# Optimization experiments

Measured on AMD Instinct MI355X. Metric: run time of the kernel, lower is better.

The kernel has to match this reference:

```python
import jax, jax.numpy as jnp
import numpy as np

EMB = 768
HEADS = 12
HEAD_DIM = EMB // HEADS
LAMBDA_INIT = 0.5
LN_EPS = 1e-5


def _rope_tables(seq_len, head_dim):
    # theta_j = 10000^{-2j/d}, j = 0..d/2-1 (standard RoPE)
    j = jnp.arange(head_dim // 2, dtype=jnp.float32)
    theta = jnp.power(10000.0, -2.0 * j / head_dim)            # [d/2]
    ang = jnp.arange(seq_len, dtype=jnp.float32)[:, None] * theta[None, :]  # [S, d/2]
    return jnp.cos(ang), jnp.sin(ang)


def _apply_rope(x, cos, sin):
    # x: [B, H, S, D]; cos/sin: [S, D/2]; rotate consecutive pairs (2j, 2j+1)
    x1 = x[..., 0::2]
    x2 = x[..., 1::2]
    c = cos[None, None, :, :]
    s = sin[None, None, :, :]
    r1 = x1 * c - x2 * s
    r2 = x1 * s + x2 * c
    return jnp.stack([r1, r2], axis=-1).reshape(x.shape)


def setup_inputs() -> dict:
    key = jax.random.key(0)
    ks = jax.random.split(key, 10)
    B, S, E = 2, 2048, EMB
    sd = 1.0 / np.sqrt(E)
    return {
        "x": jax.random.normal(ks[0], (B, S, E), jnp.float32),
        "Wq": jax.random.normal(ks[1], (E, 2 * E), jnp.float32) * sd,
        "bq": jnp.zeros((2 * E,), jnp.float32),
        "Wk": jax.random.normal(ks[2], (E, 2 * E), jnp.float32) * sd,
        "bk": jnp.zeros((2 * E,), jnp.float32),
        "Wv": jax.random.normal(ks[3], (E, E), jnp.float32) * sd,
        "bv": jnp.zeros((E,), jnp.float32),
        "Wo": jax.random.normal(ks[4], (E, E), jnp.float32) * sd,
        "bo": jnp.zeros((E,), jnp.float32),
        "q_scale": jnp.ones((1, 1, 2 * E), jnp.float32),
        "k_scale": jnp.ones((1, 1, 2 * E), jnp.float32),
        "v_scale": jnp.ones((1, 1, E), jnp.float32),
        "o_scale": jnp.ones((1, 1, E), jnp.float32),
        "lambda_param": jnp.asarray(0.0, jnp.float32),
    }


def reference(x, Wq, bq, Wk, bk, Wv, bv, Wo, bo,
              q_scale, k_scale, v_scale, o_scale, lambda_param):
    B, S, E = x.shape
    H, D = HEADS, HEAD_DIM

    Q = (x @ Wq + bq) * q_scale          # [B, S, 2E]
    K = (x @ Wk + bk) * k_scale          # [B, S, 2E]
    V = (x @ Wv + bv) * v_scale          # [B, S, E]

    Q1, Q2 = jnp.split(Q, 2, axis=-1)
    K1, K2 = jnp.split(K, 2, axis=-1)

    def to_heads(t):  # [B, S, E] -> [B, H, S, D]
        return t.reshape(B, S, H, D).transpose(0, 2, 1, 3)

    Q1, Q2, K1, K2, Vh = map(to_heads, (Q1, Q2, K1, K2, V))

    cos, sin = _rope_tables(S, D)
    Q1, Q2 = _apply_rope(Q1, cos, sin), _apply_rope(Q2, cos, sin)
    K1, K2 = _apply_rope(K1, cos, sin), _apply_rope(K2, cos, sin)

    scale = 1.0 / jnp.sqrt(jnp.asarray(D, jnp.float32))
    p1 = jax.nn.softmax(jnp.einsum("bhqd,bhkd->bhqk", Q1, K1) * scale, axis=-1)
    p2 = jax.nn.softmax(jnp.einsum("bhqd,bhkd->bhqk", Q2, K2) * scale, axis=-1)

    lam = jax.nn.sigmoid(lambda_param)
    ctx = jnp.einsum("bhqk,bhkd->bhqd", p1 - lam * p2, Vh)  # [B, H, S, D]

    # layer_norm over head_dim, no affine params
    mu = jnp.mean(ctx, axis=-1, keepdims=True)
    var = jnp.mean(jnp.square(ctx - mu), axis=-1, keepdims=True)
    ctx = (ctx - mu) * jax.lax.rsqrt(var + LN_EPS)

    ctx = ctx * (1.0 - LAMBDA_INIT)
    ctx = ctx.transpose(0, 2, 1, 3).reshape(B, S, E)
    return (ctx @ Wo + bo) * o_scale
```

## Files before the change

### kernel.cpp

```cpp
#include <hip/hip_runtime.h>
#include <hip/hip_bf16.h>

#define BB 2
#define SS 2048
#define EE 768
#define HH 12
#define DD 64
#define MM (BB*SS)

typedef __bf16 bf16_t;
typedef __bf16 bf16x8 __attribute__((ext_vector_type(8)));
typedef __bf16 bf16x4 __attribute__((ext_vector_type(4)));
typedef float  f32x4  __attribute__((ext_vector_type(4)));

static __device__ __forceinline__ f32x4 mfma16(bf16x8 a, bf16x8 b, f32x4 c) {
    return __builtin_amdgcn_mfma_f32_16x16x32_bf16(a, b, c, 0, 0, 0);
}

static __device__ __forceinline__ void gload_lds16(const bf16_t* g, bf16_t* l) {
    __builtin_amdgcn_global_load_lds(
        (const __attribute__((address_space(1))) void*)g,
        (__attribute__((address_space(3))) void*)l,
        16, 0, 0);
}

__global__ __launch_bounds__(256)
void prep_kernel(const float* __restrict__ x,
                 const float* __restrict__ Wq, const float* __restrict__ Wk,
                 const float* __restrict__ Wv, const float* __restrict__ Wo,
                 bf16_t* __restrict__ xb,
                 bf16_t* __restrict__ WqT, bf16_t* __restrict__ WkT,
                 bf16_t* __restrict__ WvT, bf16_t* __restrict__ WoT,
                 float* __restrict__ ctab, float* __restrict__ stab)
{
    __shared__ float tile[32][33];
    const int bx = blockIdx.x, tid = threadIdx.x;

    if (bx < 1536) {
        int i = (bx * 256 + tid) * 8;
        float4 a = *reinterpret_cast<const float4*>(x + i);
        float4 b = *reinterpret_cast<const float4*>(x + i + 4);
        bf16x8 v;
        v[0] = (bf16_t)a.x; v[1] = (bf16_t)a.y; v[2] = (bf16_t)a.z; v[3] = (bf16_t)a.w;
        v[4] = (bf16_t)b.x; v[5] = (bf16_t)b.y; v[6] = (bf16_t)b.z; v[7] = (bf16_t)b.w;
        *reinterpret_cast<bf16x8*>(xb + i) = v;
        return;
    }
    if (bx < 1792) {
        int t = (bx - 1536) * 256 + tid;
        int s = t >> 5, j = t & 31;
        float theta = exp2f(-(float)j * (13.287712379549449f / 32.0f));
        float ang = (float)s * theta;
        float sn, cs;
        sincosf(ang, &sn, &cs);
        ctab[t] = cs;
        stab[t] = sn;
        return;
    }
    int idx = bx - 1792;
    const float* W; bf16_t* WT; int N;
    if (idx < 1152)      { W = Wq; WT = WqT; N = 1536; }
    else if (idx < 2304) { W = Wk; WT = WkT; N = 1536; idx -= 1152; }
    else if (idx < 2880) { W = Wv; WT = WvT; N = 768;  idx -= 2304; }
    else                 { W = Wo; WT = WoT; N = 768;  idx -= 2880; }
    const int ntiles = N >> 5;
    const int n0 = (idx % ntiles) * 32, k0 = (idx / ntiles) * 32;
    const int tx = tid & 31, ty = tid >> 5;
    #pragma unroll
    for (int r = 0; r < 32; r += 8)
        tile[ty + r][tx] = W[(size_t)(k0 + ty + r) * N + n0 + tx];
    __syncthreads();
    #pragma unroll
    for (int r = 0; r < 32; r += 8)
        WT[(size_t)(n0 + ty + r) * 768 + k0 + tx] = (bf16_t)tile[tx][ty + r];
}

__global__ __launch_bounds__(256)
void gemm_qkv_kernel(const bf16_t* __restrict__ xb,
                     const bf16_t* __restrict__ WqT, const bf16_t* __restrict__ WkT,
                     const bf16_t* __restrict__ WvT,
                     const float* __restrict__ bq, const float* __restrict__ bk,
                     const float* __restrict__ bv,
                     const float* __restrict__ qs, const float* __restrict__ ks,
                     const float* __restrict__ vs,
                     const float* __restrict__ ctab, const float* __restrict__ stab,
                     bf16_t* __restrict__ Qr, bf16_t* __restrict__ Kr, bf16_t* __restrict__ Vt)
{
    __shared__ __align__(16) bf16_t As[128 * 64];
    __shared__ __align__(16) bf16_t Bs[128 * 64];
    const int tid = threadIdx.x;
    const int w = tid >> 6, lane = tid & 63, q15 = lane & 15, g = lane >> 4;
    const int m0 = blockIdx.x * 128;
    const int nt = blockIdx.y;

    const bf16_t* Wsrc; const float* bias; const float* scale;
    int nloc0, mode; bf16_t* dstQK = nullptr; float qmul = 1.0f;
    if (nt < 12)      { Wsrc = WqT; bias = bq; scale = qs; nloc0 = nt * 128;        mode = 0; dstQK = Qr;
                        qmul = 0.125f * 1.4426950408889634f; }
    else if (nt < 24) { Wsrc = WkT; bias = bk; scale = ks; nloc0 = (nt - 12) * 128; mode = 0; dstQK = Kr; }
    else              { Wsrc = WvT; bias = bv; scale = vs; nloc0 = (nt - 24) * 128; mode = 1; }

    f32x4 acc[4][4];
    #pragma unroll
    for (int i = 0; i < 4; ++i)
        #pragma unroll
        for (int j = 0; j < 4; ++j)
            acc[i][j] = f32x4{0.f, 0.f, 0.f, 0.f};

    const bf16_t* gA[4]; const bf16_t* gB[4]; bf16_t* lA[4]; bf16_t* lB[4];
    #pragma unroll
    for (int c = 0; c < 4; ++c) {
        int t16 = c * 256 + tid;
        int row = t16 >> 3;
        int sc16 = (t16 & 7) ^ (row & 7);
        gA[c] = &xb[(size_t)(m0 + row) * 768 + sc16 * 8];
        gB[c] = &Wsrc[(size_t)(nloc0 + row) * 768 + sc16 * 8];
        lA[c] = &As[(c * 256 + w * 64) * 8];
        lB[c] = &Bs[(c * 256 + w * 64) * 8];
    }

    const int ar0 = (w >> 1) * 64, bc0 = (w & 1) * 64;
    const int xr = q15 & 7;

    for (int k0 = 0; k0 < 768; k0 += 64) {
        if (k0) __syncthreads();
        #pragma unroll
        for (int c = 0; c < 4; ++c) {
            gload_lds16(gA[c] + k0, lA[c]);
            gload_lds16(gB[c] + k0, lB[c]);
        }
        __syncthreads();
        #pragma unroll
        for (int st = 0; st < 2; ++st) {
            const int cA = ((4 * st + g) ^ xr) * 8;
            bf16x8 af[4], bfr[4];
            #pragma unroll
            for (int i = 0; i < 4; ++i)
                af[i] = *reinterpret_cast<const bf16x8*>(&As[(ar0 + i * 16 + q15) * 64 + cA]);
            #pragma unroll
            for (int j = 0; j < 4; ++j)
                bfr[j] = *reinterpret_cast<const bf16x8*>(&Bs[(bc0 + j * 16 + q15) * 64 + cA]);
            #pragma unroll
            for (int i = 0; i < 4; ++i)
                #pragma unroll
                for (int j = 0; j < 4; ++j)
                    acc[i][j] = mfma16(af[i], bfr[j], acc[i][j]);
        }
    }

    const int mbase = m0 + (w >> 1) * 64;
    const int nbase = nloc0 + (w & 1) * 64;
    #pragma unroll
    for (int j = 0; j < 4; ++j) {
        const int n = nbase + j * 16 + q15;
        const float bi = bias[n];
        const float sc = scale[n] * qmul;
        if (mode == 1) {
            const int h = n >> 6, d = n & 63;
            #pragma unroll
            for (int i = 0; i < 4; ++i)
                #pragma unroll
                for (int r = 0; r < 4; ++r) {
                    int m = mbase + i * 16 + g * 4 + r;
                    int b = m >> 11, s = m & 2047;
                    float v = (acc[i][j][r] + bi) * sc;
                    Vt[((size_t)(b * HH + h) * DD + d) * SS + s] = (bf16_t)v;
                }
        } else {
            const int br = (n >= 768) ? 1 : 0;
            const int n2 = n - br * 768;
            const int h = n2 >> 6, d = n2 & 63, jj = d >> 1;
            #pragma unroll
            for (int i = 0; i < 4; ++i)
                #pragma unroll
                for (int r = 0; r < 4; ++r) {
                    int m = mbase + i * 16 + g * 4 + r;
                    int b = m >> 11, s = m & 2047;
                    float v = (acc[i][j][r] + bi) * sc;
                    float p = __shfl_xor(v, 1);
                    float cs = ctab[s * 32 + jj], sn = stab[s * 32 + jj];
                    float outv = (d & 1) ? (p * sn + v * cs) : (v * cs - p * sn);
                    dstQK[(((size_t)(b * 2 + br) * HH + h) * SS + s) * DD + d] = (bf16_t)outv;
                }
        }
    }
}

__global__ __launch_bounds__(256)
void attn_kernel(const bf16_t* __restrict__ Qr, const bf16_t* __restrict__ Kr,
                 const bf16_t* __restrict__ Vt, const float* __restrict__ lambda_param,
                 bf16_t* __restrict__ ctx)
{
    __shared__ __align__(16) char smem[27648];
    bf16_t (*K1s)[72] = (bf16_t (*)[72])(smem);
    bf16_t (*K2s)[72] = (bf16_t (*)[72])(smem + 9216);
    bf16_t (*Vs)[72]  = (bf16_t (*)[72])(smem + 18432);
    float  (*Cb)[68]  = (float  (*)[68])(smem);

    const int bh = blockIdx.y, b = bh / HH, h = bh % HH;
    const int s0 = blockIdx.x * 64;
    const int tid = threadIdx.x, w = tid >> 6, lane = tid & 63, q15 = lane & 15, g = lane >> 4;
    const int br = w >> 1, half = w & 1;

    const bf16_t* Qp = Qr + (((size_t)(b * 2 + br) * HH + h) * SS + (s0 + half * 32 + q15)) * DD;
    bf16x8 qf[2][2];
    #pragma unroll
    for (int j = 0; j < 2; ++j)
        #pragma unroll
        for (int st = 0; st < 2; ++st)
            qf[j][st] = *reinterpret_cast<const bf16x8*>(Qp + (size_t)j * 16 * DD + st * 32 + g * 8);

    const bf16_t* K1base = Kr + ((size_t)(b * 2 + 0) * HH + h) * SS * DD;
    const bf16_t* K2base = Kr + ((size_t)(b * 2 + 1) * HH + h) * SS * DD;
    const bf16_t* Vbase  = Vt + ((size_t)b * HH + h) * DD * SS;

    f32x4 lacc[2];
    f32x4 O[2][4];
    #pragma unroll
    for (int j = 0; j < 2; ++j) {
        lacc[j] = f32x4{0.f, 0.f, 0.f, 0.f};
        #pragma unroll
        for (int df = 0; df < 4; ++df)
            O[j][df] = f32x4{0.f, 0.f, 0.f, 0.f};
    }
    bf16x8 onesv;
    #pragma unroll
    for (int e = 0; e < 8; ++e) onesv[e] = (bf16_t)1.0f;

    const int srow = tid >> 3, scol = (tid & 7) * 8;
    const int u0 = (scol & 32) + ((scol & 15) >> 2) * 8 + ((scol >> 4) & 1) * 4;

    const bf16_t (*Ksb)[72] = br ? K2s : K1s;

    bf16x8 rK1[2], rK2[2], rV[2];
    #pragma unroll
    for (int ii = 0; ii < 2; ++ii) {
        int r2 = srow + ii * 32;
        rK1[ii] = *reinterpret_cast<const bf16x8*>(&K1base[(size_t)r2 * DD + scol]);
        rK2[ii] = *reinterpret_cast<const bf16x8*>(&K2base[(size_t)r2 * DD + scol]);
        rV[ii]  = *reinterpret_cast<const bf16x8*>(&Vbase[(size_t)r2 * SS + scol]);
    }

    for (int kb = 0; kb < SS; kb += 64) {
        if (kb) __syncthreads();
        #pragma unroll
        for (int ii = 0; ii < 2; ++ii) {
            int r2 = srow + ii * 32;
            *reinterpret_cast<bf16x8*>(&K1s[r2][scol]) = rK1[ii];
            *reinterpret_cast<bf16x8*>(&K2s[r2][scol]) = rK2[ii];
            bf16x4 lo = __builtin_shufflevector(rV[ii], rV[ii], 0, 1, 2, 3);
            bf16x4 hi = __builtin_shufflevector(rV[ii], rV[ii], 4, 5, 6, 7);
            *reinterpret_cast<bf16x4*>(&Vs[r2][u0])     = lo;
            *reinterpret_cast<bf16x4*>(&Vs[r2][u0 + 8]) = hi;
        }
        __syncthreads();
        if (kb + 64 < SS) {
            int kn = kb + 64;
            #pragma unroll
            for (int ii = 0; ii < 2; ++ii) {
                int r2 = srow + ii * 32;
                rK1[ii] = *reinterpret_cast<const bf16x8*>(&K1base[(size_t)(kn + r2) * DD + scol]);
                rK2[ii] = *reinterpret_cast<const bf16x8*>(&K2base[(size_t)(kn + r2) * DD + scol]);
                rV[ii]  = *reinterpret_cast<const bf16x8*>(&Vbase[(size_t)r2 * SS + kn + scol]);
            }
        }

        f32x4 sf[2][4];
        #pragma unroll
        for (int rf = 0; rf < 4; ++rf) {
            bf16x8 kf0 = *reinterpret_cast<const bf16x8*>(&Ksb[rf * 16 + q15][g * 8]);
            bf16x8 kf1 = *reinterpret_cast<const bf16x8*>(&Ksb[rf * 16 + q15][32 + g * 8]);
            #pragma unroll
            for (int j = 0; j < 2; ++j) {
                f32x4 a = mfma16(kf0, qf[j][0], f32x4{0.f, 0.f, 0.f, 0.f});
                sf[j][rf] = mfma16(kf1, qf[j][1], a);
            }
        }

        bf16x8 pa[2][2];
        #pragma unroll
        for (int j = 0; j < 2; ++j)
            #pragma unroll
            for (int st = 0; st < 2; ++st)
                #pragma unroll
                for (int e = 0; e < 8; ++e)
                    pa[j][st][e] = (bf16_t)__builtin_amdgcn_exp2f(sf[j][st * 2 + (e >> 2)][e & 3]);

        #pragma unroll
        for (int j = 0; j < 2; ++j) {
            lacc[j] = mfma16(pa[j][0], onesv, lacc[j]);
            lacc[j] = mfma16(pa[j][1], onesv, lacc[j]);
        }

        #pragma unroll
        for (int df = 0; df < 4; ++df) {
            bf16x8 vf0 = *reinterpret_cast<const bf16x8*>(&Vs[df * 16 + q15][g * 8]);
            bf16x8 vf1 = *reinterpret_cast<const bf16x8*>(&Vs[df * 16 + q15][32 + g * 8]);
            #pragma unroll
            for (int j = 0; j < 2; ++j) {
                O[j][df] = mfma16(pa[j][0], vf0, O[j][df]);
                O[j][df] = mfma16(pa[j][1], vf1, O[j][df]);
            }
        }
    }

    __syncthreads();

    if (br == 1) {
        const float lam = 1.0f / (1.0f + __expf(-lambda_param[0]));
        #pragma unroll
        for (int j = 0; j < 2; ++j) {
            #pragma unroll
            for (int r = 0; r < 4; ++r) {
                float inv = lam / lacc[j][r];
                int lq = half * 32 + j * 16 + g * 4 + r;
                #pragma unroll
                for (int df = 0; df < 4; ++df)
                    Cb[lq][df * 16 + q15] = O[j][df][r] * inv;
            }
        }
    }
    __syncthreads();

    if (br == 0) {
        #pragma unroll
        for (int j = 0; j < 2; ++j) {
            #pragma unroll
            for (int r = 0; r < 4; ++r) {
                float inv = 1.0f / lacc[j][r];
                int lq = half * 32 + j * 16 + g * 4 + r;
                float cv[4];
                #pragma unroll
                for (int df = 0; df < 4; ++df)
                    cv[df] = O[j][df][r] * inv - Cb[lq][df * 16 + q15];
                float sum = cv[0] + cv[1] + cv[2] + cv[3];
                sum += __shfl_xor(sum, 1); sum += __shfl_xor(sum, 2);
                sum += __shfl_xor(sum, 4); sum += __shfl_xor(sum, 8);
                float mu = sum * (1.0f / 64.0f);
                float vac = 0.f;
                #pragma unroll
                for (int df = 0; df < 4; ++df) { float dv = cv[df] - mu; vac += dv * dv; }
                vac += __shfl_xor(vac, 1); vac += __shfl_xor(vac, 2);
                vac += __shfl_xor(vac, 4); vac += __shfl_xor(vac, 8);
                float rs = rsqrtf(vac * (1.0f / 64.0f) + 1e-5f);
                int s = s0 + lq;
                size_t rowoff = ((size_t)b * SS + s) * EE + h * DD;
                #pragma unroll
                for (int df = 0; df < 4; ++df)
                    ctx[rowoff + df * 16 + q15] = (bf16_t)((cv[df] - mu) * rs * 0.5f);
            }
        }
    }
}

__global__ __launch_bounds__(256)
void gemm_out_kernel(const bf16_t* __restrict__ ctxb, const bf16_t* __restrict__ WoT,
                     const float* __restrict__ bo, const float* __restrict__ os,
                     float* __restrict__ out)
{
    __shared__ __align__(16) bf16_t As[64 * 64];
    __shared__ __align__(16) bf16_t Bs[128 * 64];
    const int tid = threadIdx.x;
    const int w = tid >> 6, lane = tid & 63, q15 = lane & 15, g = lane >> 4;
    const int m0 = blockIdx.x * 64;
    const int nloc0 = blockIdx.y * 128;

    f32x4 acc[2][4];
    #pragma unroll
    for (int i = 0; i < 2; ++i)
        #pragma unroll
        for (int j = 0; j < 4; ++j)
            acc[i][j] = f32x4{0.f, 0.f, 0.f, 0.f};

    const bf16_t* gA[2]; const bf16_t* gB[4]; bf16_t* lA[2]; bf16_t* lB[4];
    #pragma unroll
    for (int c = 0; c < 2; ++c) {
        int t16 = c * 256 + tid;
        int row = t16 >> 3;
        int sc16 = (t16 & 7) ^ (row & 7);
        gA[c] = &ctxb[(size_t)(m0 + row) * 768 + sc16 * 8];
        lA[c] = &As[(c * 256 + w * 64) * 8];
    }
    #pragma unroll
    for (int c = 0; c < 4; ++c) {
        int t16 = c * 256 + tid;
        int row = t16 >> 3;
        int sc16 = (t16 & 7) ^ (row & 7);
        gB[c] = &WoT[(size_t)(nloc0 + row) * 768 + sc16 * 8];
        lB[c] = &Bs[(c * 256 + w * 64) * 8];
    }

    const int ar0 = (w >> 1) * 32, bc0 = (w & 1) * 64;
    const int xr = q15 & 7;

    for (int k0 = 0; k0 < 768; k0 += 64) {
        if (k0) __syncthreads();
        #pragma unroll
        for (int c = 0; c < 2; ++c) gload_lds16(gA[c] + k0, lA[c]);
        #pragma unroll
        for (int c = 0; c < 4; ++c) gload_lds16(gB[c] + k0, lB[c]);
        __syncthreads();
        #pragma unroll
        for (int st = 0; st < 2; ++st) {
            const int cA = ((4 * st + g) ^ xr) * 8;
            bf16x8 af[2], bfr[4];
            #pragma unroll
            for (int i = 0; i < 2; ++i)
                af[i] = *reinterpret_cast<const bf16x8*>(&As[(ar0 + i * 16 + q15) * 64 + cA]);
            #pragma unroll
            for (int j = 0; j < 4; ++j)
                bfr[j] = *reinterpret_cast<const bf16x8*>(&Bs[(bc0 + j * 16 + q15) * 64 + cA]);
            #pragma unroll
            for (int i = 0; i < 2; ++i)
                #pragma unroll
                for (int j = 0; j < 4; ++j)
                    acc[i][j] = mfma16(af[i], bfr[j], acc[i][j]);
        }
    }

    const int mbase = m0 + (w >> 1) * 32;
    const int nbase = nloc0 + (w & 1) * 64;
    #pragma unroll
    for (int j = 0; j < 4; ++j) {
        const int n = nbase + j * 16 + q15;
        const float bi = bo[n], sc = os[n];
        #pragma unroll
        for (int i = 0; i < 2; ++i)
            #pragma unroll
            for (int r = 0; r < 4; ++r) {
                int m = mbase + i * 16 + g * 4 + r;
                out[(size_t)m * 768 + n] = (acc[i][j][r] + bi) * sc;
            }
    }
}

extern "C" void kernel_launch(void* const* d_in, const int* in_sizes, int n_in,
                              void* d_out, int out_size, void* d_ws, size_t ws_size,
                              hipStream_t stream)
{
    (void)in_sizes; (void)n_in; (void)out_size; (void)ws_size;
    const float* x  = (const float*)d_in[0];
    const float* Wq = (const float*)d_in[1];
    const float* bq = (const float*)d_in[2];
    const float* Wk = (const float*)d_in[3];
    const float* bk = (const float*)d_in[4];
    const float* Wv = (const float*)d_in[5];
    const float* bv = (const float*)d_in[6];
    const float* Wo = (const float*)d_in[7];
    const float* bo = (const float*)d_in[8];
    const float* qs = (const float*)d_in[9];
    const float* ks = (const float*)d_in[10];
    const float* vs = (const float*)d_in[11];
    const float* os = (const float*)d_in[12];
    const float* lp = (const float*)d_in[13];
    float* out = (float*)d_out;

    char* ws = (char*)d_ws;
    bf16_t* xb   = (bf16_t*)(ws);
    bf16_t* WqT  = (bf16_t*)(ws + 6291456);
    bf16_t* WkT  = (bf16_t*)(ws + 8650752);
    bf16_t* WvT  = (bf16_t*)(ws + 11010048);
    bf16_t* WoT  = (bf16_t*)(ws + 12189696);
    bf16_t* Qr   = (bf16_t*)(ws + 13369344);
    bf16_t* Kr   = (bf16_t*)(ws + 25952256);
    bf16_t* Vt   = (bf16_t*)(ws + 38535168);
    bf16_t* ctxb = (bf16_t*)(ws + 44826624);
    float*  ctab = (float*)(ws + 51118080);
    float*  stab = (float*)(ws + 51380224);

    prep_kernel<<<dim3(5248), dim3(256), 0, stream>>>(x, Wq, Wk, Wv, Wo,
                                                      xb, WqT, WkT, WvT, WoT, ctab, stab);
    gemm_qkv_kernel<<<dim3(32, 30), dim3(256), 0, stream>>>(xb, WqT, WkT, WvT,
                                                            bq, bk, bv, qs, ks, vs,
                                                            ctab, stab, Qr, Kr, Vt);
    attn_kernel<<<dim3(32, 24), dim3(256), 0, stream>>>(Qr, Kr, Vt, lp, ctxb);
    gemm_out_kernel<<<dim3(64, 6), dim3(256), 0, stream>>>(ctxb, WoT, bo, os, out);
}
```

Measured before the change: 128.1 us.

## Stage V transpose through LDS for coalesced stores; remap attention blocks per XCD

```diff
diff --git a/kernel.cpp b/kernel.cpp
--- a/kernel.cpp
+++ b/kernel.cpp
@@ -86,8 +86,9 @@
                      const float* __restrict__ ctab, const float* __restrict__ stab,
                      bf16_t* __restrict__ Qr, bf16_t* __restrict__ Kr, bf16_t* __restrict__ Vt)
 {
-    __shared__ __align__(16) bf16_t As[128 * 64];
-    __shared__ __align__(16) bf16_t Bs[128 * 64];
+    __shared__ __align__(16) bf16_t sm[17408];
+    bf16_t* As = sm;
+    bf16_t* Bs = sm + 8192;
     const int tid = threadIdx.x;
     const int w = tid >> 6, lane = tid & 63, q15 = lane & 15, g = lane >> 4;
     const int m0 = blockIdx.x * 128;
@@ -150,39 +151,54 @@
 
     const int mbase = m0 + (w >> 1) * 64;
     const int nbase = nloc0 + (w & 1) * 64;
+
+    if (mode == 1) {
+        __syncthreads();
+        #pragma unroll
+        for (int j = 0; j < 4; ++j) {
+            const int nl = (w & 1) * 64 + j * 16 + q15;
+            const int n = nloc0 + nl;
+            const float bi = bias[n], sc = scale[n];
+            #pragma unroll
+            for (int i = 0; i < 4; ++i) {
+                const int ml = (w >> 1) * 64 + i * 16 + g * 4;
+                #pragma unroll
+                for (int r = 0; r < 4; ++r)
+                    sm[nl * 136 + ml + r] = (bf16_t)((acc[i][j][r] + bi) * sc);
+            }
+        }
+        __syncthreads();
+        const int nl = tid >> 1, mh = (tid & 1) * 64;
+        const int n = nloc0 + nl, h = n >> 6, d = n & 63;
+        const int b = m0 >> 11, sbase = (m0 & 2047) + mh;
+        bf16_t* dst = Vt + ((size_t)(b * HH + h) * DD + d) * SS + sbase;
+        #pragma unroll
+        for (int c = 0; c < 8; ++c)
+            *reinterpret_cast<bf16x8*>(dst + c * 8) =
+                *reinterpret_cast<const bf16x8*>(&sm[nl * 136 + mh + c * 8]);
+        return;
+    }
+
     #pragma unroll
     for (int j = 0; j < 4; ++j) {
         const int n = nbase + j * 16 + q15;
         const float bi = bias[n];
         const float sc = scale[n] * qmul;
-        if (mode == 1) {
-            const int h = n >> 6, d = n & 63;
-            #pragma unroll
-            for (int i = 0; i < 4; ++i)
-                #pragma unroll
-                for (int r = 0; r < 4; ++r) {
-                    int m = mbase + i * 16 + g * 4 + r;
-                    int b = m >> 11, s = m & 2047;
-                    float v = (acc[i][j][r] + bi) * sc;
-                    Vt[((size_t)(b * HH + h) * DD + d) * SS + s] = (bf16_t)v;
-                }
-        } else {
-            const int br = (n >= 768) ? 1 : 0;
-            const int n2 = n - br * 768;
-            const int h = n2 >> 6, d = n2 & 63, jj = d >> 1;
-            #pragma unroll
-            for (int i = 0; i < 4; ++i)
-                #pragma unroll
-                for (int r = 0; r < 4; ++r) {
-                    int m = mbase + i * 16 + g * 4 + r;
-                    int b = m >> 11, s = m & 2047;
-                    float v = (acc[i][j][r] + bi) * sc;
-                    float p = __shfl_xor(v, 1);
-                    float cs = ctab[s * 32 + jj], sn = stab[s * 32 + jj];
-                    float outv = (d & 1) ? (p * sn + v * cs) : (v * cs - p * sn);
-                    dstQK[(((size_t)(b * 2 + br) * HH + h) * SS + s) * DD + d] = (bf16_t)outv;
-                }
-        }
+        const int br = (n >= 768) ? 1 : 0;
+        const int n2 = n - br * 768;
+        const int h = n2 >> 6, d = n2 & 63, jj = d >> 1;
+        #pragma unroll
+        for (int i = 0; i < 4; ++i)
+            #pragma unroll
+            for (int r = 0; r < 4; ++r) {
+                int m = mbase + i * 16 + g * 4 + r;
+                int b = m >> 11, s = m & 2047;
+                float v = (acc[i][j][r] + bi) * sc;
+                float p = __shfl_xor(v, 1);
+                float cs = ctab[s * 32 + jj], sn = stab[s * 32 + jj];
+                float outv = (d & 1) ? (p * sn + v * cs) : (v * cs - p * sn);
+                dstQK[(((size_t)(b * 2 + br) * HH + h) * SS + s) * DD + d] = (bf16_t)outv;
+            }
     }
 }
 
@@ -197,8 +213,10 @@
     bf16_t (*Vs)[72]  = (bf16_t (*)[72])(smem + 18432);
     float  (*Cb)[68]  = (float  (*)[68])(smem);
 
-    const int bh = blockIdx.y, b = bh / HH, h = bh % HH;
-    const int s0 = blockIdx.x * 64;
+    const int idlin = blockIdx.x;
+    const int work = ((idlin & 7) * 96) + (idlin >> 3);
+    const int bh = work >> 5, b = bh / HH, h = bh % HH;
+    const int s0 = (work & 31) * 64;
     const int tid = threadIdx.x, w = tid >> 6, lane = tid & 63, q15 = lane & 15, g = lane >> 4;
     const int br = w >> 1, half = w & 1;
 
@@ -473,6 +491,6 @@
     gemm_qkv_kernel<<<dim3(32, 30), dim3(256), 0, stream>>>(xb, WqT, WkT, WvT,
                                                             bq, bk, bv, qs, ks, vs,
                                                             ctab, stab, Qr, Kr, Vt);
-    attn_kernel<<<dim3(32, 24), dim3(256), 0, stream>>>(Qr, Kr, Vt, lp, ctxb);
+    attn_kernel<<<dim3(768), dim3(256), 0, stream>>>(Qr, Kr, Vt, lp, ctxb);
     gemm_out_kernel<<<dim3(64, 6), dim3(256), 0, stream>>>(ctxb, WoT, bo, os, out);
 }
```

Result: no change. 126.1 us (median of 2 runs) (-1.5%).
